# Kernel tuning notes

Measured on AMD Instinct MI355X. Metric: run time of the kernel, lower is better.

The kernel has to match this reference:

```python
import jax, jax.numpy as jnp
import numpy as np

B, H_HIST, S_DIM, HID, G, K, A = 1024, 16384, 32, 64, 10, 4, 8


def setup_inputs() -> dict:
    key = jax.random.key(0)
    ks = jax.random.split(key, 12)
    inp = {
        'state_batch': jax.random.normal(ks[0], (B, S_DIM), jnp.float32),
        'state_history_batch': jax.random.normal(ks[1], (H_HIST, S_DIM), jnp.float32),
        'joint_action_history_batch': jax.random.normal(ks[2], (H_HIST, G, A), jnp.float32),
        # per-abstract-agent encoder MLP: Linear(S->H) + ReLU, Linear(H->H) + ReLU, Linear(H->H) + ReLU
        'W0': jax.random.normal(ks[3], (K, S_DIM, HID), jnp.float32) / np.sqrt(S_DIM),
        'b0': jax.random.normal(ks[4], (K, HID), jnp.float32) * 0.01,
        'W1': jax.random.normal(ks[5], (K, HID, HID), jnp.float32) / np.sqrt(HID),
        'b1': jax.random.normal(ks[6], (K, HID), jnp.float32) * 0.01,
        'W2': jax.random.normal(ks[7], (K, HID, HID), jnp.float32) / np.sqrt(HID),
        'b2': jax.random.normal(ks[8], (K, HID), jnp.float32) * 0.01,
        'assignment_matrix': jnp.ones((G, K), jnp.float32),
    }
    return inp


def _encode(x, W0, b0, W1, b1, W2, b2):
    # x: [N, S_DIM] shared across K encoders -> [K, N, HID]
    h = jax.nn.relu(jnp.einsum('ni,kio->kno', x, W0) + b0[:, None, :])
    h = jax.nn.relu(jnp.einsum('kni,kio->kno', h, W1) + b1[:, None, :])
    h = jax.nn.relu(jnp.einsum('kni,kio->kno', h, W2) + b2[:, None, :])
    return h


def reference(state_batch, state_history_batch, joint_action_history_batch,
              W0, b0, W1, b1, W2, b2, assignment_matrix):
    enc_s = _encode(state_batch, W0, b0, W1, b1, W2, b2)            # [K, B, HID]
    enc_h = _encode(state_history_batch, W0, b0, W1, b1, W2, b2)    # [K, H, HID]
    # per (abstract agent k, batch item b): softmax over history of <enc_h, enc_s>
    attn = jax.nn.softmax(jnp.einsum('khd,kbd->kbh', enc_h, enc_s), axis=-1)  # [K, B, H]
    # weighted action aggregation: [H,G,A] contracted over H
    abs_pred = jnp.einsum('kbh,hga->kbga', attn, joint_action_history_batch)  # [K, B, G, A]
    soft_assign = jax.nn.softmax(assignment_matrix, axis=-1)                  # [G, K]
    out = jnp.einsum('gk,kbga->bga', soft_assign, abs_pred)                   # [B, G, A]
    return out
```

## Files before the change

### kernel.cpp

```cpp
#include <hip/hip_runtime.h>
#include <stdint.h>

#define B_SZ 1024
#define H_SZ 16384
#define SD   32
#define HID  64
#define G_SZ 10
#define K_SZ 4
#define A_SZ 8
#define VA   80
#define NC   16
#define CH   (H_SZ/NC)

typedef float f32x4  __attribute__((ext_vector_type(4)));
typedef short bf16x8 __attribute__((ext_vector_type(8)));

__device__ inline short f2bf(float a) {
    unsigned u = __float_as_uint(a);
    return (short)((u + 0x7FFFu + ((u >> 16) & 1u)) >> 16);
}
__device__ inline float bf2f(short s) {
    return __uint_as_float(((unsigned)(unsigned short)s) << 16);
}
__device__ inline void split_bf(float v, short& hi, short& lo) {
    hi = f2bf(v);
    lo = f2bf(v - bf2f(hi));
}
__device__ inline int pk_bf16(float a, float b) {
    unsigned ua = __float_as_uint(a), ub = __float_as_uint(b);
    ua = (ua + 0x7FFFu + ((ua >> 16) & 1u)) >> 16;
    ub = (ub + 0x7FFFu + ((ub >> 16) & 1u)) >> 16;
    return (int)(ua | (ub << 16));
}

__global__ __launch_bounds__(256, 2) void k_encode(
    const float* __restrict__ state, const float* __restrict__ hist,
    const float* __restrict__ act,
    const float* __restrict__ W0, const float* __restrict__ b0,
    const float* __restrict__ W1, const float* __restrict__ b1,
    const float* __restrict__ W2, const float* __restrict__ b2,
    short* __restrict__ enc_s_h, short* __restrict__ enc_s_l,
    short* __restrict__ enc_h_h, short* __restrict__ enc_h_l,
    short* __restrict__ vt_h, short* __restrict__ vt_l)
{
    __shared__ __align__(16) short smem[28672];
    const int bid = blockIdx.x;
    const int t = threadIdx.x;

    if (bid >= 1088) {
        short* tile_h = smem;
        short* tile_l = smem + 10752;
        const int h0 = (bid - 1088) * 128;
        for (int i = 0; i < 40; ++i) {
            int idx = t + i * 256;
            float v = act[(size_t)h0 * VA + idx];
            int h = idx / VA, c = idx - h * VA;
            short hh, ll; split_bf(v, hh, ll);
            tile_h[h * 84 + c] = hh;
            tile_l[h * 84 + c] = ll;
        }
        __syncthreads();
        for (int i = 0; i < 5; ++i) {
            int j = t + i * 256;
            int va = j >> 4, hc = j & 15;
            union { short s[8]; uint4 v; } uh, ul;
            #pragma unroll
            for (int uu = 0; uu < 8; ++uu) {
                uh.s[uu] = tile_h[(hc * 8 + uu) * 84 + va];
                ul.s[uu] = tile_l[(hc * 8 + uu) * 84 + va];
            }
            *(uint4*)(vt_h + (size_t)va * H_SZ + h0 + hc * 8) = uh.v;
            *(uint4*)(vt_l + (size_t)va * H_SZ + h0 + hc * 8) = ul.v;
        }
        return;
    }

    const int k = bid / 272;
    const int tl = bid % 272;
    const float* X;
    short *dst_h, *dst_l;
    if (tl < 16) {
        X = state + (size_t)tl * 64 * SD;
        dst_h = enc_s_h + ((size_t)k * B_SZ + tl * 64) * HID;
        dst_l = enc_s_l + ((size_t)k * B_SZ + tl * 64) * HID;
    } else {
        X = hist + (size_t)(tl - 16) * 64 * SD;
        dst_h = enc_h_h + ((size_t)k * H_SZ + (tl - 16) * 64) * HID;
        dst_l = enc_h_l + ((size_t)k * H_SZ + (tl - 16) * 64) * HID;
    }

    short* xt_h  = smem;
    short* xt_l  = smem + 2560;
    short* wt0_h = smem + 5120;
    short* wt0_l = smem + 7680;
    short* hb2_h = smem;
    short* hb2_l = smem + 4608;
    short* wt1_h = smem + 10240;
    short* wt1_l = smem + 14848;
    short* hb1_h = smem + 19456;
    short* hb1_l = smem + 24064;
    short* wt2_h = smem + 19456;
    short* wt2_l = smem + 24064;

    const float* W0k = W0 + k * (SD * HID);
    const float* W1k = W1 + k * (HID * HID);
    const float* W2k = W2 + k * (HID * HID);

    {
        int r = t >> 2, c0 = (t & 3) * 8;
        const float* src = X + r * SD + c0;
        #pragma unroll
        for (int u = 0; u < 8; ++u) {
            short hh, ll; split_bf(src[u], hh, ll);
            xt_h[r * 40 + c0 + u] = hh;
            xt_l[r * 40 + c0 + u] = ll;
        }
    }
    {
        int i = t >> 3, j0 = (t & 7) * 8;
        #pragma unroll
        for (int u = 0; u < 8; ++u) {
            short hh, ll; split_bf(W0k[i * HID + j0 + u], hh, ll);
            wt0_h[(j0 + u) * 40 + i] = hh;
            wt0_l[(j0 + u) * 40 + i] = ll;
        }
    }
    {
        int i = t >> 2, j0 = (t & 3) * 16;
        #pragma unroll
        for (int u = 0; u < 16; ++u) {
            short hh, ll; split_bf(W1k[i * HID + j0 + u], hh, ll);
            wt1_h[(j0 + u) * 72 + i] = hh;
            wt1_l[(j0 + u) * 72 + i] = ll;
        }
    }
    __syncthreads();

    const int w = t >> 6, l15 = t & 15, quad = (t >> 4) & 3;
    const f32x4 fz = {0.f, 0.f, 0.f, 0.f};

    {
        bf16x8 xa_h = *(const bf16x8*)(xt_h + (w * 16 + l15) * 40 + quad * 8);
        bf16x8 xa_l = *(const bf16x8*)(xt_l + (w * 16 + l15) * 40 + quad * 8);
        const float* b0k = b0 + k * HID;
        #pragma unroll
        for (int tt = 0; tt < 4; ++tt) {
            bf16x8 wf_h = *(const bf16x8*)(wt0_h + (l15 + 16 * tt) * 40 + quad * 8);
            bf16x8 wf_l = *(const bf16x8*)(wt0_l + (l15 + 16 * tt) * 40 + quad * 8);
            f32x4 c = __builtin_amdgcn_mfma_f32_16x16x32_bf16(xa_h, wf_h, fz, 0, 0, 0);
            c = __builtin_amdgcn_mfma_f32_16x16x32_bf16(xa_l, wf_h, c, 0, 0, 0);
            c = __builtin_amdgcn_mfma_f32_16x16x32_bf16(xa_h, wf_l, c, 0, 0, 0);
            float bias = b0k[l15 + 16 * tt];
            #pragma unroll
            for (int r = 0; r < 4; ++r) {
                float f = fmaxf(c[r] + bias, 0.f);
                short hh, ll; split_bf(f, hh, ll);
                hb1_h[(w * 16 + quad * 4 + r) * 72 + l15 + 16 * tt] = hh;
                hb1_l[(w * 16 + quad * 4 + r) * 72 + l15 + 16 * tt] = ll;
            }
        }
    }
    __syncthreads();
    {
        bf16x8 ha0_h = *(const bf16x8*)(hb1_h + (w * 16 + l15) * 72 + quad * 8);
        bf16x8 ha0_l = *(const bf16x8*)(hb1_l + (w * 16 + l15) * 72 + quad * 8);
        bf16x8 ha1_h = *(const bf16x8*)(hb1_h + (w * 16 + l15) * 72 + 32 + quad * 8);
        bf16x8 ha1_l = *(const bf16x8*)(hb1_l + (w * 16 + l15) * 72 + 32 + quad * 8);
        const float* b1k = b1 + k * HID;
        #pragma unroll
        for (int tt = 0; tt < 4; ++tt) {
            bf16x8 wfa_h = *(const bf16x8*)(wt1_h + (l15 + 16 * tt) * 72 + quad * 8);
            bf16x8 wfa_l = *(const bf16x8*)(wt1_l + (l15 + 16 * tt) * 72 + quad * 8);
            bf16x8 wfb_h = *(const bf16x8*)(wt1_h + (l15 + 16 * tt) * 72 + 32 + quad * 8);
            bf16x8 wfb_l = *(const bf16x8*)(wt1_l + (l15 + 16 * tt) * 72 + 32 + quad * 8);
            f32x4 c = __builtin_amdgcn_mfma_f32_16x16x32_bf16(ha0_h, wfa_h, fz, 0, 0, 0);
            c = __builtin_amdgcn_mfma_f32_16x16x32_bf16(ha1_h, wfb_h, c, 0, 0, 0);
            c = __builtin_amdgcn_mfma_f32_16x16x32_bf16(ha0_l, wfa_h, c, 0, 0, 0);
            c = __builtin_amdgcn_mfma_f32_16x16x32_bf16(ha1_l, wfb_h, c, 0, 0, 0);
            c = __builtin_amdgcn_mfma_f32_16x16x32_bf16(ha0_h, wfa_l, c, 0, 0, 0);
            c = __builtin_amdgcn_mfma_f32_16x16x32_bf16(ha1_h, wfb_l, c, 0, 0, 0);
            float bias = b1k[l15 + 16 * tt];
            #pragma unroll
            for (int r = 0; r < 4; ++r) {
                float f = fmaxf(c[r] + bias, 0.f);
                short hh, ll; split_bf(f, hh, ll);
                hb2_h[(w * 16 + quad * 4 + r) * 72 + l15 + 16 * tt] = hh;
                hb2_l[(w * 16 + quad * 4 + r) * 72 + l15 + 16 * tt] = ll;
            }
        }
    }
    __syncthreads();
    {
        int i = t >> 2, j0 = (t & 3) * 16;
        #pragma unroll
        for (int u = 0; u < 16; ++u) {
            short hh, ll; split_bf(W2k[i * HID + j0 + u], hh, ll);
            wt2_h[(j0 + u) * 72 + i] = hh;
            wt2_l[(j0 + u) * 72 + i] = ll;
        }
    }
    __syncthreads();
    {
        bf16x8 ha0_h = *(const bf16x8*)(hb2_h + (w * 16 + l15) * 72 + quad * 8);
        bf16x8 ha0_l = *(const bf16x8*)(hb2_l + (w * 16 + l15) * 72 + quad * 8);
        bf16x8 ha1_h = *(const bf16x8*)(hb2_h + (w * 16 + l15) * 72 + 32 + quad * 8);
        bf16x8 ha1_l = *(const bf16x8*)(hb2_l + (w * 16 + l15) * 72 + 32 + quad * 8);
        const float* b2k = b2 + k * HID;
        #pragma unroll
        for (int tt = 0; tt < 4; ++tt) {
            bf16x8 wfa_h = *(const bf16x8*)(wt2_h + (l15 + 16 * tt) * 72 + quad * 8);
            bf16x8 wfa_l = *(const bf16x8*)(wt2_l + (l15 + 16 * tt) * 72 + quad * 8);
            bf16x8 wfb_h = *(const bf16x8*)(wt2_h + (l15 + 16 * tt) * 72 + 32 + quad * 8);
            bf16x8 wfb_l = *(const bf16x8*)(wt2_l + (l15 + 16 * tt) * 72 + 32 + quad * 8);
            f32x4 c = __builtin_amdgcn_mfma_f32_16x16x32_bf16(ha0_h, wfa_h, fz, 0, 0, 0);
            c = __builtin_amdgcn_mfma_f32_16x16x32_bf16(ha1_h, wfb_h, c, 0, 0, 0);
            c = __builtin_amdgcn_mfma_f32_16x16x32_bf16(ha0_l, wfa_h, c, 0, 0, 0);
            c = __builtin_amdgcn_mfma_f32_16x16x32_bf16(ha1_l, wfb_h, c, 0, 0, 0);
            c = __builtin_amdgcn_mfma_f32_16x16x32_bf16(ha0_h, wfa_l, c, 0, 0, 0);
            c = __builtin_amdgcn_mfma_f32_16x16x32_bf16(ha1_h, wfb_l, c, 0, 0, 0);
            float bias = b2k[l15 + 16 * tt];
            #pragma unroll
            for (int r = 0; r < 4; ++r) {
                float f = fmaxf(c[r] + bias, 0.f);
                short hh, ll; split_bf(f, hh, ll);
                dst_h[(w * 16 + quad * 4 + r) * HID + l15 + 16 * tt] = hh;
                dst_l[(w * 16 + quad * 4 + r) * HID + l15 + 16 * tt] = ll;
            }
        }
    }
}

__global__ __launch_bounds__(256, 2) void k_flash(
    const short* __restrict__ enc_s_h, const short* __restrict__ enc_s_l,
    const short* __restrict__ enc_h_h, const short* __restrict__ enc_h_l,
    const short* __restrict__ vth, const short* __restrict__ vtl,
    float* __restrict__ Pm, float* __restrict__ Pl, float* __restrict__ Pacc)
{
    __shared__ __align__(16) short kh_h[32 * 72];
    __shared__ __align__(16) short kh_l[32 * 72];
    __shared__ __align__(16) short vts_h[80 * 40];
    __shared__ __align__(16) short vts_l[80 * 40];

    const int bid = blockIdx.x;
    const int mtile = bid & 7, chunk = (bid >> 3) & 15, k = bid >> 7;
    const int t = threadIdx.x, w = t >> 6, l15 = t & 15, quad = (t >> 4) & 3;
    const short* ehk_h = enc_h_h + (size_t)k * H_SZ * HID;
    const short* ehk_l = enc_h_l + (size_t)k * H_SZ * HID;
    const int h_base = chunk * CH;
    const int q0 = mtile * 128 + w * 32;
    const float L2E = 1.44269504f;
    const f32x4 fz = {0.f, 0.f, 0.f, 0.f};

    bf16x8 qh[2][2], ql[2][2];
    #pragma unroll
    for (int sub = 0; sub < 2; ++sub)
        #pragma unroll
        for (int kb = 0; kb < 2; ++kb) {
            size_t off = ((size_t)k * B_SZ + q0 + sub * 16 + l15) * HID + kb * 32 + quad * 8;
            qh[sub][kb] = *(const bf16x8*)(enc_s_h + off);
            ql[sub][kb] = *(const bf16x8*)(enc_s_l + off);
        }

    f32x4 acc[2][5];
    #pragma unroll
    for (int s = 0; s < 2; ++s)
        #pragma unroll
        for (int tt = 0; tt < 5; ++tt) acc[s][tt] = fz;
    float mrun[2] = {-__builtin_inff(), -__builtin_inff()};
    float lrun[2] = {0.f, 0.f};

    const int krr = t >> 3, kcc = (t & 7) * 8;
    const int vrw = t >> 2, vcl = (t & 3) * 8;
    const int vrw2 = 64 + (t >> 2);

    uint4 pkh, pkl, pvh, pvl, pv2h, pv2l;
    auto load_tile = [&](int h0) {
        pkh = *(const uint4*)(ehk_h + (size_t)(h0 + krr) * HID + kcc);
        pkl = *(const uint4*)(ehk_l + (size_t)(h0 + krr) * HID + kcc);
        pvh = *(const uint4*)(vth + (size_t)vrw * H_SZ + h0 + vcl);
        pvl = *(const uint4*)(vtl + (size_t)vrw * H_SZ + h0 + vcl);
        if (t < 64) {
            pv2h = *(const uint4*)(vth + (size_t)vrw2 * H_SZ + h0 + vcl);
            pv2l = *(const uint4*)(vtl + (size_t)vrw2 * H_SZ + h0 + vcl);
        }
    };
    auto store_tile = [&]() {
        *(uint4*)(kh_h + krr * 72 + kcc) = pkh;
        *(uint4*)(kh_l + krr * 72 + kcc) = pkl;
        *(uint4*)(vts_h + vrw * 40 + vcl) = pvh;
        *(uint4*)(vts_l + vrw * 40 + vcl) = pvl;
        if (t < 64) {
            *(uint4*)(vts_h + vrw2 * 40 + vcl) = pv2h;
            *(uint4*)(vts_l + vrw2 * 40 + vcl) = pv2l;
        }
    };

    load_tile(h_base);
    store_tile();

    for (int it = 0; it < CH / 32; ++it) {
        const int h0 = h_base + it * 32;
        __syncthreads();
        if (it + 1 < CH / 32) load_tile(h0 + 32);

        bf16x8 ka_h[2][2], ka_l[2][2];
        #pragma unroll
        for (int hs = 0; hs < 2; ++hs)
            #pragma unroll
            for (int kb = 0; kb < 2; ++kb) {
                ka_h[hs][kb] = *(const bf16x8*)(kh_h + (hs * 16 + l15) * 72 + kb * 32 + quad * 8);
                ka_l[hs][kb] = *(const bf16x8*)(kh_l + (hs * 16 + l15) * 72 + kb * 32 + quad * 8);
            }

        bf16x8 pfv[2];
        #pragma unroll
        for (int sub = 0; sub < 2; ++sub) {
            f32x4 slo = __builtin_amdgcn_mfma_f32_16x16x32_bf16(ka_h[0][0], qh[sub][0], fz, 0, 0, 0);
            slo = __builtin_amdgcn_mfma_f32_16x16x32_bf16(ka_h[0][1], qh[sub][1], slo, 0, 0, 0);
            slo = __builtin_amdgcn_mfma_f32_16x16x32_bf16(ka_l[0][0], qh[sub][0], slo, 0, 0, 0);
            slo = __builtin_amdgcn_mfma_f32_16x16x32_bf16(ka_l[0][1], qh[sub][1], slo, 0, 0, 0);
            slo = __builtin_amdgcn_mfma_f32_16x16x32_bf16(ka_h[0][0], ql[sub][0], slo, 0, 0, 0);
            slo = __builtin_amdgcn_mfma_f32_16x16x32_bf16(ka_h[0][1], ql[sub][1], slo, 0, 0, 0);
            f32x4 shi = __builtin_amdgcn_mfma_f32_16x16x32_bf16(ka_h[1][0], qh[sub][0], fz, 0, 0, 0);
            shi = __builtin_amdgcn_mfma_f32_16x16x32_bf16(ka_h[1][1], qh[sub][1], shi, 0, 0, 0);
            shi = __builtin_amdgcn_mfma_f32_16x16x32_bf16(ka_l[1][0], qh[sub][0], shi, 0, 0, 0);
            shi = __builtin_amdgcn_mfma_f32_16x16x32_bf16(ka_l[1][1], qh[sub][1], shi, 0, 0, 0);
            shi = __builtin_amdgcn_mfma_f32_16x16x32_bf16(ka_h[1][0], ql[sub][0], shi, 0, 0, 0);
            shi = __builtin_amdgcn_mfma_f32_16x16x32_bf16(ka_h[1][1], ql[sub][1], shi, 0, 0, 0);

            float tm = fmaxf(fmaxf(fmaxf(slo[0], slo[1]), fmaxf(slo[2], slo[3])),
                             fmaxf(fmaxf(shi[0], shi[1]), fmaxf(shi[2], shi[3])));
            tm = fmaxf(tm, __shfl_xor(tm, 16));
            tm = fmaxf(tm, __shfl_xor(tm, 32));
            float mnew = fmaxf(mrun[sub], tm);
            float alpha = exp2f((mrun[sub] - mnew) * L2E);
            float p0 = exp2f((slo[0] - mnew) * L2E), p1 = exp2f((slo[1] - mnew) * L2E);
            float p2 = exp2f((slo[2] - mnew) * L2E), p3 = exp2f((slo[3] - mnew) * L2E);
            float p4 = exp2f((shi[0] - mnew) * L2E), p5 = exp2f((shi[1] - mnew) * L2E);
            float p6 = exp2f((shi[2] - mnew) * L2E), p7 = exp2f((shi[3] - mnew) * L2E);
            float ps = (p0 + p1) + (p2 + p3) + (p4 + p5) + (p6 + p7);
            ps += __shfl_xor(ps, 16);
            ps += __shfl_xor(ps, 32);
            lrun[sub] = lrun[sub] * alpha + ps;
            mrun[sub] = mnew;
            #pragma unroll
            for (int tt = 0; tt < 5; ++tt) acc[sub][tt] = acc[sub][tt] * alpha;

            int plo01 = pk_bf16(p0, p1), plo23 = pk_bf16(p2, p3);
            int phi01 = pk_bf16(p4, p5), phi23 = pk_bf16(p6, p7);
            union { int i[4]; bf16x8 v; } pf;
            #pragma unroll
            for (int jj = 0; jj < 4; ++jj) {
                int src = (((2 * quad + (jj >> 1)) & 3) << 4) + l15;
                int glo = __shfl((jj & 1) ? plo23 : plo01, src);
                int ghi = __shfl((jj & 1) ? phi23 : phi01, src);
                pf.i[jj] = (quad >= 2) ? ghi : glo;
            }
            pfv[sub] = pf.v;
        }

        #pragma unroll
        for (int tt = 0; tt < 5; ++tt) {
            bf16x8 vh = *(const bf16x8*)(vts_h + (l15 + 16 * tt) * 40 + quad * 8);
            bf16x8 vl = *(const bf16x8*)(vts_l + (l15 + 16 * tt) * 40 + quad * 8);
            acc[0][tt] = __builtin_amdgcn_mfma_f32_16x16x32_bf16(vh, pfv[0], acc[0][tt], 0, 0, 0);
            acc[0][tt] = __builtin_amdgcn_mfma_f32_16x16x32_bf16(vl, pfv[0], acc[0][tt], 0, 0, 0);
            acc[1][tt] = __builtin_amdgcn_mfma_f32_16x16x32_bf16(vh, pfv[1], acc[1][tt], 0, 0, 0);
            acc[1][tt] = __builtin_amdgcn_mfma_f32_16x16x32_bf16(vl, pfv[1], acc[1][tt], 0, 0, 0);
        }

        __syncthreads();
        if (it + 1 < CH / 32) store_tile();
    }

    const int qg = k * B_SZ + q0;
    #pragma unroll
    for (int sub = 0; sub < 2; ++sub) {
        int q = qg + sub * 16 + l15;
        if (quad == 0) {
            Pm[chunk * 4096 + q] = mrun[sub];
            Pl[chunk * 4096 + q] = lrun[sub];
        }
        #pragma unroll
        for (int tt = 0; tt < 5; ++tt)
            #pragma unroll
            for (int r = 0; r < 4; ++r) {
                int va = tt * 16 + quad * 4 + r;
                Pacc[((size_t)chunk * VA + va) * 4096 + q] = acc[sub][tt][r];
            }
    }
}

__global__ __launch_bounds__(256) void k_reduce1(
    const float* __restrict__ Pm, const float* __restrict__ Pl,
    const float* __restrict__ Pacc, float* __restrict__ O)
{
    const int bid = blockIdx.x;
    const int qb = bid / 5, vc = bid - qb * 5;
    const int t = threadIdx.x;
    const int q = qb * 64 + (t & 63);
    const int va0 = vc * 16 + (t >> 6) * 4;
    const float L2E = 1.44269504f;

    float mc[NC];
    float M = -__builtin_inff();
    #pragma unroll
    for (int c = 0; c < NC; ++c) { mc[c] = Pm[c * 4096 + q]; M = fmaxf(M, mc[c]); }
    float wv[NC];
    float L = 0.f;
    #pragma unroll
    for (int c = 0; c < NC; ++c) {
        wv[c] = exp2f((mc[c] - M) * L2E);
        L += wv[c] * Pl[c * 4096 + q];
    }
    float inv = 1.f / L;
    float o[4] = {0.f, 0.f, 0.f, 0.f};
    #pragma unroll
    for (int c = 0; c < NC; ++c) {
        #pragma unroll
        for (int j = 0; j < 4; ++j)
            o[j] += wv[c] * Pacc[((size_t)c * VA + va0 + j) * 4096 + q];
    }
    #pragma unroll
    for (int j = 0; j < 4; ++j)
        O[(size_t)q * VA + va0 + j] = o[j] * inv;
}

__global__ __launch_bounds__(256) void k_reduce2(
    const float* __restrict__ O, const float* __restrict__ assign,
    float* __restrict__ out)
{
    const int idx = blockIdx.x * 256 + threadIdx.x;
    const int b = idx / VA, va = idx - b * VA, g = va >> 3;
    const float L2E = 1.44269504f;
    float a0 = assign[g * K_SZ + 0], a1 = assign[g * K_SZ + 1];
    float a2 = assign[g * K_SZ + 2], a3 = assign[g * K_SZ + 3];
    float mx = fmaxf(fmaxf(a0, a1), fmaxf(a2, a3));
    float e0 = exp2f((a0 - mx) * L2E), e1 = exp2f((a1 - mx) * L2E);
    float e2 = exp2f((a2 - mx) * L2E), e3 = exp2f((a3 - mx) * L2E);
    float inv = 1.f / (e0 + e1 + e2 + e3);
    float o = e0 * O[((size_t)(0 * B_SZ + b)) * VA + va]
            + e1 * O[((size_t)(1 * B_SZ + b)) * VA + va]
            + e2 * O[((size_t)(2 * B_SZ + b)) * VA + va]
            + e3 * O[((size_t)(3 * B_SZ + b)) * VA + va];
    out[idx] = o * inv;
}

extern "C" void kernel_launch(void* const* d_in, const int* in_sizes, int n_in,
                              void* d_out, int out_size, void* d_ws, size_t ws_size,
                              hipStream_t stream)
{
    const float* state  = (const float*)d_in[0];
    const float* hist   = (const float*)d_in[1];
    const float* act    = (const float*)d_in[2];
    const float* W0     = (const float*)d_in[3];
    const float* b0     = (const float*)d_in[4];
    const float* W1     = (const float*)d_in[5];
    const float* b1     = (const float*)d_in[6];
    const float* W2     = (const float*)d_in[7];
    const float* b2     = (const float*)d_in[8];
    const float* assign = (const float*)d_in[9];
    float* out = (float*)d_out;

    char* ws = (char*)d_ws;
    short* enc_s_h = (short*)(ws);
    short* enc_s_l = (short*)(ws + 524288);
    short* enc_h_h = (short*)(ws + 1048576);
    short* enc_h_l = (short*)(ws + 9437184);
    short* vt_h    = (short*)(ws + 17825792);
    short* vt_l    = (short*)(ws + 20447232);
    float* Pm      = (float*)(ws + 23068672);
    float* Pl      = (float*)(ws + 23330816);
    float* Pacc    = (float*)(ws + 23592960);
    float* O       = (float*)(ws + 44564480);

    k_encode<<<1216, 256, 0, stream>>>(state, hist, act, W0, b0, W1, b1, W2, b2,
                                       enc_s_h, enc_s_l, enc_h_h, enc_h_l, vt_h, vt_l);
    k_flash<<<512, 256, 0, stream>>>(enc_s_h, enc_s_l, enc_h_h, enc_h_l, vt_h, vt_l,
                                     Pm, Pl, Pacc);
    k_reduce1<<<320, 256, 0, stream>>>(Pm, Pl, Pacc, O);
    k_reduce2<<<320, 256, 0, stream>>>(O, assign, out);
}
```

Measured before the change: 177.5 us.

## Double split-K chunks, skip unneeded rescales, raise MFMA priority, widen reduce grid

```diff
diff --git a/kernel.cpp b/kernel.cpp
--- a/kernel.cpp
+++ b/kernel.cpp
@@ -9,8 +9,6 @@
 #define K_SZ 4
 #define A_SZ 8
 #define VA   80
-#define NC   16
-#define CH   (H_SZ/NC)
 
 typedef float f32x4  __attribute__((ext_vector_type(4)));
 typedef short bf16x8 __attribute__((ext_vector_type(8)));
@@ -230,23 +228,25 @@
     }
 }
 
-__global__ __launch_bounds__(256, 2) void k_flash(
+template<int NCt>
+__global__ __launch_bounds__(256, 4) void k_flash(
     const short* __restrict__ enc_s_h, const short* __restrict__ enc_s_l,
     const short* __restrict__ enc_h_h, const short* __restrict__ enc_h_l,
     const short* __restrict__ vth, const short* __restrict__ vtl,
     float* __restrict__ Pm, float* __restrict__ Pl, float* __restrict__ Pacc)
 {
+    constexpr int CHt = H_SZ / NCt;
     __shared__ __align__(16) short kh_h[32 * 72];
     __shared__ __align__(16) short kh_l[32 * 72];
     __shared__ __align__(16) short vts_h[80 * 40];
     __shared__ __align__(16) short vts_l[80 * 40];
 
     const int bid = blockIdx.x;
-    const int mtile = bid & 7, chunk = (bid >> 3) & 15, k = bid >> 7;
+    const int mtile = bid & 7, chunk = (bid >> 3) & (NCt - 1), k = bid / (8 * NCt);
     const int t = threadIdx.x, w = t >> 6, l15 = t & 15, quad = (t >> 4) & 3;
     const short* ehk_h = enc_h_h + (size_t)k * H_SZ * HID;
     const short* ehk_l = enc_h_l + (size_t)k * H_SZ * HID;
-    const int h_base = chunk * CH;
+    const int h_base = chunk * CHt;
     const int q0 = mtile * 128 + w * 32;
     const float L2E = 1.44269504f;
     const f32x4 fz = {0.f, 0.f, 0.f, 0.f};
@@ -298,10 +298,10 @@
     load_tile(h_base);
     store_tile();
 
-    for (int it = 0; it < CH / 32; ++it) {
+    for (int it = 0; it < CHt / 32; ++it) {
         const int h0 = h_base + it * 32;
         __syncthreads();
-        if (it + 1 < CH / 32) load_tile(h0 + 32);
+        if (it + 1 < CHt / 32) load_tile(h0 + 32);
 
         bf16x8 ka_h[2][2], ka_l[2][2];
         #pragma unroll
@@ -315,6 +315,7 @@
         bf16x8 pfv[2];
         #pragma unroll
         for (int sub = 0; sub < 2; ++sub) {
+            __builtin_amdgcn_s_setprio(1);
             f32x4 slo = __builtin_amdgcn_mfma_f32_16x16x32_bf16(ka_h[0][0], qh[sub][0], fz, 0, 0, 0);
             slo = __builtin_amdgcn_mfma_f32_16x16x32_bf16(ka_h[0][1], qh[sub][1], slo, 0, 0, 0);
             slo = __builtin_amdgcn_mfma_f32_16x16x32_bf16(ka_l[0][0], qh[sub][0], slo, 0, 0, 0);
@@ -327,24 +328,29 @@
             shi = __builtin_amdgcn_mfma_f32_16x16x32_bf16(ka_l[1][1], qh[sub][1], shi, 0, 0, 0);
             shi = __builtin_amdgcn_mfma_f32_16x16x32_bf16(ka_h[1][0], ql[sub][0], shi, 0, 0, 0);
             shi = __builtin_amdgcn_mfma_f32_16x16x32_bf16(ka_h[1][1], ql[sub][1], shi, 0, 0, 0);
+            __builtin_amdgcn_s_setprio(0);
 
             float tm = fmaxf(fmaxf(fmaxf(slo[0], slo[1]), fmaxf(slo[2], slo[3])),
                              fmaxf(fmaxf(shi[0], shi[1]), fmaxf(shi[2], shi[3])));
             tm = fmaxf(tm, __shfl_xor(tm, 16));
             tm = fmaxf(tm, __shfl_xor(tm, 32));
-            float mnew = fmaxf(mrun[sub], tm);
-            float alpha = exp2f((mrun[sub] - mnew) * L2E);
-            float p0 = exp2f((slo[0] - mnew) * L2E), p1 = exp2f((slo[1] - mnew) * L2E);
-            float p2 = exp2f((slo[2] - mnew) * L2E), p3 = exp2f((slo[3] - mnew) * L2E);
-            float p4 = exp2f((shi[0] - mnew) * L2E), p5 = exp2f((shi[1] - mnew) * L2E);
-            float p6 = exp2f((shi[2] - mnew) * L2E), p7 = exp2f((shi[3] - mnew) * L2E);
+            if (__any(tm > mrun[sub])) {
+                float mnew = fmaxf(mrun[sub], tm);
+                float alpha = exp2f((mrun[sub] - mnew) * L2E);
+                lrun[sub] *= alpha;
+                #pragma unroll
+                for (int tt = 0; tt < 5; ++tt) acc[sub][tt] = acc[sub][tt] * alpha;
+                mrun[sub] = mnew;
+            }
+            float m = mrun[sub];
+            float p0 = exp2f((slo[0] - m) * L2E), p1 = exp2f((slo[1] - m) * L2E);
+            float p2 = exp2f((slo[2] - m) * L2E), p3 = exp2f((slo[3] - m) * L2E);
+            float p4 = exp2f((shi[0] - m) * L2E), p5 = exp2f((shi[1] - m) * L2E);
+            float p6 = exp2f((shi[2] - m) * L2E), p7 = exp2f((shi[3] - m) * L2E);
             float ps = (p0 + p1) + (p2 + p3) + (p4 + p5) + (p6 + p7);
             ps += __shfl_xor(ps, 16);
             ps += __shfl_xor(ps, 32);
-            lrun[sub] = lrun[sub] * alpha + ps;
-            mrun[sub] = mnew;
-            #pragma unroll
-            for (int tt = 0; tt < 5; ++tt) acc[sub][tt] = acc[sub][tt] * alpha;
+            lrun[sub] += ps;
 
             int plo01 = pk_bf16(p0, p1), plo23 = pk_bf16(p2, p3);
             int phi01 = pk_bf16(p4, p5), phi23 = pk_bf16(p6, p7);
@@ -359,6 +365,7 @@
             pfv[sub] = pf.v;
         }
 
+        __builtin_amdgcn_s_setprio(1);
         #pragma unroll
         for (int tt = 0; tt < 5; ++tt) {
             bf16x8 vh = *(const bf16x8*)(vts_h + (l15 + 16 * tt) * 40 + quad * 8);
@@ -368,9 +375,10 @@
             acc[1][tt] = __builtin_amdgcn_mfma_f32_16x16x32_bf16(vh, pfv[1], acc[1][tt], 0, 0, 0);
             acc[1][tt] = __builtin_amdgcn_mfma_f32_16x16x32_bf16(vl, pfv[1], acc[1][tt], 0, 0, 0);
         }
+        __builtin_amdgcn_s_setprio(0);
 
         __syncthreads();
-        if (it + 1 < CH / 32) store_tile();
+        if (it + 1 < CHt / 32) store_tile();
     }
 
     const int qg = k * B_SZ + q0;
@@ -391,39 +399,34 @@
     }
 }
 
+template<int NCt>
 __global__ __launch_bounds__(256) void k_reduce1(
     const float* __restrict__ Pm, const float* __restrict__ Pl,
     const float* __restrict__ Pacc, float* __restrict__ O)
 {
     const int bid = blockIdx.x;
-    const int qb = bid / 5, vc = bid - qb * 5;
+    const int qb = bid / 10, vc = bid - qb * 10;
     const int t = threadIdx.x;
     const int q = qb * 64 + (t & 63);
-    const int va0 = vc * 16 + (t >> 6) * 4;
+    const int va0 = vc * 8 + (t >> 6) * 2;
     const float L2E = 1.44269504f;
 
-    float mc[NC];
+    float mc[NCt];
     float M = -__builtin_inff();
     #pragma unroll
-    for (int c = 0; c < NC; ++c) { mc[c] = Pm[c * 4096 + q]; M = fmaxf(M, mc[c]); }
-    float wv[NC];
+    for (int c = 0; c < NCt; ++c) { mc[c] = Pm[c * 4096 + q]; M = fmaxf(M, mc[c]); }
     float L = 0.f;
+    float o0 = 0.f, o1 = 0.f;
     #pragma unroll
-    for (int c = 0; c < NC; ++c) {
-        wv[c] = exp2f((mc[c] - M) * L2E);
-        L += wv[c] * Pl[c * 4096 + q];
+    for (int c = 0; c < NCt; ++c) {
+        float wv = exp2f((mc[c] - M) * L2E);
+        L += wv * Pl[c * 4096 + q];
+        o0 += wv * Pacc[((size_t)c * VA + va0) * 4096 + q];
+        o1 += wv * Pacc[((size_t)c * VA + va0 + 1) * 4096 + q];
     }
     float inv = 1.f / L;
-    float o[4] = {0.f, 0.f, 0.f, 0.f};
-    #pragma unroll
-    for (int c = 0; c < NC; ++c) {
-        #pragma unroll
-        for (int j = 0; j < 4; ++j)
-            o[j] += wv[c] * Pacc[((size_t)c * VA + va0 + j) * 4096 + q];
-    }
-    #pragma unroll
-    for (int j = 0; j < 4; ++j)
-        O[(size_t)q * VA + va0 + j] = o[j] * inv;
+    O[(size_t)q * VA + va0]     = o0 * inv;
+    O[(size_t)q * VA + va0 + 1] = o1 * inv;
 }
 
 __global__ __launch_bounds__(256) void k_reduce2(
@@ -469,15 +472,26 @@
     short* enc_h_l = (short*)(ws + 9437184);
     short* vt_h    = (short*)(ws + 17825792);
     short* vt_l    = (short*)(ws + 20447232);
-    float* Pm      = (float*)(ws + 23068672);
-    float* Pl      = (float*)(ws + 23330816);
-    float* Pacc    = (float*)(ws + 23592960);
-    float* O       = (float*)(ws + 44564480);
+    const size_t base = 23068672;
+
+    const size_t need32 = base + 32ull * (32768 + 1310720) + 1310720;
+    const int nc = (ws_size >= need32) ? 32 : 16;
+
+    float* Pm   = (float*)(ws + base);
+    float* Pl   = (float*)(ws + base + (size_t)nc * 16384);
+    float* Pacc = (float*)(ws + base + (size_t)nc * 32768);
+    float* O    = (float*)(ws + base + (size_t)nc * 32768 + (size_t)nc * 1310720);
 
     k_encode<<<1216, 256, 0, stream>>>(state, hist, act, W0, b0, W1, b1, W2, b2,
                                        enc_s_h, enc_s_l, enc_h_h, enc_h_l, vt_h, vt_l);
-    k_flash<<<512, 256, 0, stream>>>(enc_s_h, enc_s_l, enc_h_h, enc_h_l, vt_h, vt_l,
-                                     Pm, Pl, Pacc);
-    k_reduce1<<<320, 256, 0, stream>>>(Pm, Pl, Pacc, O);
+    if (nc == 32) {
+        k_flash<32><<<1024, 256, 0, stream>>>(enc_s_h, enc_s_l, enc_h_h, enc_h_l,
+                                              vt_h, vt_l, Pm, Pl, Pacc);
+        k_reduce1<32><<<640, 256, 0, stream>>>(Pm, Pl, Pacc, O);
+    } else {
+        k_flash<16><<<512, 256, 0, stream>>>(enc_s_h, enc_s_l, enc_h_h, enc_h_l,
+                                             vt_h, vt_l, Pm, Pl, Pacc);
+        k_reduce1<16><<<640, 256, 0, stream>>>(Pm, Pl, Pacc, O);
+    }
     k_reduce2<<<320, 256, 0, stream>>>(O, assign, out);
 }
```

New measurement: 261.6 us. +47.4%, slower.
